# Kernel tuning notes

Hardware: AMD Instinct MI355X
Metric: run time of the kernel (lower is better)

Reference implementation:

```python
import jax, jax.numpy as jnp
import numpy as np

K = 2          # kernel_size
DEPTH = 4
NQ = 4         # n_qubits = max(K*K, DEPTH)
B, C, H, W = 32, 3, 128, 128
LAYERS = 4     # circuit_layers


def setup_inputs() -> dict:
    key = jax.random.key(0)
    k1, k2 = jax.random.split(key)
    x = jax.random.uniform(k1, (B, C, H, W), dtype=jnp.float32)
    # TorchLayer default init is uniform in [0, 2*pi)
    weights = jax.random.uniform(k2, (LAYERS, NQ), dtype=jnp.float32) * (2.0 * np.pi)
    return {"x": x, "weights": weights}


def _apply_ry(state, theta, q):
    # state: [N,2,2,2,2] real amplitudes; theta: scalar; RY = [[c,-s],[s,c]], c=cos(t/2), s=sin(t/2)
    c = jnp.cos(theta / 2)
    s = jnp.sin(theta / 2)
    ax = 1 + q
    a0 = jnp.take(state, 0, axis=ax)
    a1 = jnp.take(state, 1, axis=ax)
    return jnp.stack([c * a0 - s * a1, s * a0 + c * a1], axis=ax)


def _cnot(state, ctrl, tgt):
    # flip target axis on the control=1 slab
    ca, ta = 1 + ctrl, 1 + tgt
    s0 = jnp.take(state, 0, axis=ca)
    s1 = jnp.take(state, 1, axis=ca)
    ta2 = ta - 1 if ta > ca else ta  # axis shift after take removed ca
    s1 = jnp.flip(s1, axis=ta2)
    return jnp.stack([s0, s1], axis=ca)


def reference(x, weights):
    Bx, Cx, Hx, Wx = x.shape
    R = Hx - K + 1  # output spatial size (H == W)
    # 2x2 patches flattened row-major, matching t.reshape(1,-1).squeeze()
    pat = jnp.stack([
        x[:, :, 0:R, 0:R], x[:, :, 0:R, 1:R + 1],
        x[:, :, 1:R + 1, 0:R], x[:, :, 1:R + 1, 1:R + 1],
    ], axis=-1)  # [B,C,R,R,4]
    half = (np.pi * pat).reshape(-1, NQ) / 2  # RY(pi*x)/2 encoding angles, [N,4]
    amp = jnp.stack([jnp.cos(half), jnp.sin(half)], axis=-1)  # [N,4,2]
    # product state over 4 qubits -> [N,2,2,2,2]
    state = jnp.einsum('na,nb,nc,nd->nabcd', amp[:, 0], amp[:, 1], amp[:, 2], amp[:, 3])
    # StructureLayer: per layer RY on all wires, then CNOT(0,1), CNOT(2,3), CNOT(1,2)
    for layer in range(weights.shape[0]):
        for q in range(NQ):
            state = _apply_ry(state, weights[layer, q], q)
        state = _cnot(state, 0, 1)
        state = _cnot(state, 2, 3)
        state = _cnot(state, 1, 2)
    probs = state * state  # amplitudes are real
    sgn = jnp.array([1.0, -1.0], dtype=state.dtype)
    z = jnp.stack([
        jnp.einsum('nabcd,a->n', probs, sgn),
        jnp.einsum('nabcd,b->n', probs, sgn),
        jnp.einsum('nabcd,c->n', probs, sgn),
        jnp.einsum('nabcd,d->n', probs, sgn),
    ], axis=-1)  # [N, DEPTH]
    q_out = z.reshape(Bx, Cx, R, R, DEPTH).sum(axis=1)  # sum over channels -> [B,R,R,DEPTH]
    # faithful to torch.reshape (memory reinterpretation, NOT a transpose)
    return q_out.reshape(Bx, DEPTH, R, R)
```

## Files before the change

### kernel.cpp

```cpp
#include <hip/hip_runtime.h>


#define BATCH   32
#define CHAN    3
#define HDIM    128
#define WDIM    128
#define RDIM    127
#define NLAYERS 4

__global__ __launch_bounds__(256) void rqcnn_kernel(
    const float* __restrict__ x,
    const float* __restrict__ w,
    float* __restrict__ out)
{
    __shared__ float cw_s[16], sw_s[16];
    const int t = threadIdx.x;
    if (t < 16) {
        float rev = w[t] * 0.07957747154594767f;
        cw_s[t] = __builtin_amdgcn_cosf(rev);
        sw_s[t] = __builtin_amdgcn_sinf(rev);
    }
    __syncthreads();

    float cw[16], sw[16];
    #pragma unroll
    for (int k = 0; k < 16; ++k) { cw[k] = cw_s[k]; sw[k] = sw_s[k]; }

    const int NPIX = BATCH * RDIM * RDIM;
    int tid = blockIdx.x * 256 + t;
    if (tid >= NPIX) return;

    int j    = tid % RDIM;
    int rest = tid / RDIM;
    int i    = rest % RDIM;
    int b    = rest / RDIM;

    float z0 = 0.f, z1 = 0.f, z2 = 0.f, z3 = 0.f;

    for (int c = 0; c < CHAN; ++c) {
        int base = ((b * CHAN + c) * HDIM + i) * WDIM + j;
        float v0 = x[base];
        float v1 = x[base + 1];
        float v2 = x[base + WDIM];
        float v3 = x[base + WDIM + 1];

        float ca0 = __builtin_amdgcn_cosf(0.25f * v0), sa0 = __builtin_amdgcn_sinf(0.25f * v0);
        float ca1 = __builtin_amdgcn_cosf(0.25f * v1), sa1 = __builtin_amdgcn_sinf(0.25f * v1);
        float ca2 = __builtin_amdgcn_cosf(0.25f * v2), sa2 = __builtin_amdgcn_sinf(0.25f * v2);
        float ca3 = __builtin_amdgcn_cosf(0.25f * v3), sa3 = __builtin_amdgcn_sinf(0.25f * v3);

        float aq[2] = {ca0, sa0};
        float bq[2] = {ca1, sa1};
        float cq[2] = {ca2, sa2};
        float dq[2] = {ca3, sa3};

        float st[16];
        #pragma unroll
        for (int ia = 0; ia < 2; ++ia) {
            #pragma unroll
            for (int ib = 0; ib < 2; ++ib) {
                float ab = aq[ia] * bq[ib];
                #pragma unroll
                for (int ic = 0; ic < 2; ++ic) {
                    float abc = ab * cq[ic];
                    #pragma unroll
                    for (int id = 0; id < 2; ++id)
                        st[ia*8 + ib*4 + ic*2 + id] = abc * dq[id];
                }
            }
        }

        #pragma unroll
        for (int l = 0; l < NLAYERS; ++l) {
            #pragma unroll
            for (int q = 0; q < 4; ++q) {
                float cc = cw[l*4 + q];
                float ss = sw[l*4 + q];
                const int m = 1 << (3 - q);
                #pragma unroll
                for (int s0 = 0; s0 < 16; ++s0) {
                    if (s0 & m) continue;
                    int s1i = s0 | m;
                    float a0 = st[s0], a1 = st[s1i];
                    st[s0]  = cc * a0 - ss * a1;
                    st[s1i] = ss * a0 + cc * a1;
                }
            }
            #pragma unroll
            for (int s0 = 0; s0 < 16; ++s0)
                if ((s0 & 8) && !(s0 & 4)) { float tmp = st[s0]; st[s0] = st[s0|4]; st[s0|4] = tmp; }
            #pragma unroll
            for (int s0 = 0; s0 < 16; ++s0)
                if ((s0 & 2) && !(s0 & 1)) { float tmp = st[s0]; st[s0] = st[s0|1]; st[s0|1] = tmp; }
            #pragma unroll
            for (int s0 = 0; s0 < 16; ++s0)
                if ((s0 & 4) && !(s0 & 2)) { float tmp = st[s0]; st[s0] = st[s0|2]; st[s0|2] = tmp; }
        }

        float p[16];
        #pragma unroll
        for (int s0 = 0; s0 < 16; ++s0) p[s0] = st[s0] * st[s0];

        float A0 = (p[0] + p[1]) + (p[2] + p[3]);
        float A1 = (p[4] + p[5]) + (p[6] + p[7]);
        float A2 = (p[8] + p[9]) + (p[10] + p[11]);
        float A3 = (p[12] + p[13]) + (p[14] + p[15]);
        float B0 = (p[0] + p[4]) + (p[8] + p[12]);
        float B1 = (p[1] + p[5]) + (p[9] + p[13]);
        float B2 = (p[2] + p[6]) + (p[10] + p[14]);
        float B3 = (p[3] + p[7]) + (p[11] + p[15]);
        z0 += (A0 + A1) - (A2 + A3);
        z1 += (A0 + A2) - (A1 + A3);
        z2 += (B0 + B1) - (B2 + B3);
        z3 += (B0 + B2) - (B1 + B3);
    }

    reinterpret_cast<float4*>(out)[tid] = make_float4(z0, z1, z2, z3);
}

extern "C" void kernel_launch(void* const* d_in, const int* in_sizes, int n_in,
                              void* d_out, int out_size, void* d_ws, size_t ws_size,
                              hipStream_t stream) {
    const float* x = (const float*)d_in[0];
    const float* w = (const float*)d_in[1];
    float* out = (float*)d_out;

    const int NPIX = BATCH * RDIM * RDIM;
    int blocks = (NPIX + 255) / 256;
    rqcnn_kernel<<<blocks, 256, 0, stream>>>(x, w, out);
}
```

Before: 78.89 us.

## Fold first RY layer into encoding angles and pack two batches per thread

The first layer's RY rotations act on a product state, so they are absorbed into the encoding angles (angle plus weight/2) and only three layers are applied explicitly. Each thread now handles two pixels from the two batch halves using 2-wide float vectors, so the compiler can emit packed FP32 math (v_pk_fma/mul) and the weight loads are amortized over twice the work. This halves the number of threads and raises register pressure per thread, which may lower occupancy.

```diff
diff --git a/kernel.cpp b/kernel.cpp
--- a/kernel.cpp
+++ b/kernel.cpp
@@ -6,63 +6,80 @@
 #define HDIM    128
 #define WDIM    128
 #define RDIM    127
-#define NLAYERS 4
+#define HALFB   16
+
+typedef float v2 __attribute__((ext_vector_type(2)));
 
 __global__ __launch_bounds__(256) void rqcnn_kernel(
     const float* __restrict__ x,
     const float* __restrict__ w,
     float* __restrict__ out)
 {
-    __shared__ float cw_s[16], sw_s[16];
+    __shared__ float cw_s[16], sw_s[16], wrev_s[4];
     const int t = threadIdx.x;
     if (t < 16) {
         float rev = w[t] * 0.07957747154594767f;
         cw_s[t] = __builtin_amdgcn_cosf(rev);
         sw_s[t] = __builtin_amdgcn_sinf(rev);
+        if (t < 4) wrev_s[t] = rev;
     }
     __syncthreads();
 
-    float cw[16], sw[16];
+    float cw[12], sw[12];
     #pragma unroll
-    for (int k = 0; k < 16; ++k) { cw[k] = cw_s[k]; sw[k] = sw_s[k]; }
+    for (int k = 0; k < 12; ++k) { cw[k] = cw_s[k + 4]; sw[k] = sw_s[k + 4]; }
+    float wr0 = wrev_s[0], wr1 = wrev_s[1], wr2 = wrev_s[2], wr3 = wrev_s[3];
 
-    const int NPIX = BATCH * RDIM * RDIM;
+    const int NHALF = HALFB * RDIM * RDIM;
     int tid = blockIdx.x * 256 + t;
-    if (tid >= NPIX) return;
+    if (tid >= NHALF) return;
 
     int j    = tid % RDIM;
     int rest = tid / RDIM;
     int i    = rest % RDIM;
     int b    = rest / RDIM;
 
-    float z0 = 0.f, z1 = 0.f, z2 = 0.f, z3 = 0.f;
+    const int XOFF = HALFB * CHAN * HDIM * WDIM;
+
+    v2 z0 = 0.f, z1 = 0.f, z2 = 0.f, z3 = 0.f;
 
     for (int c = 0; c < CHAN; ++c) {
         int base = ((b * CHAN + c) * HDIM + i) * WDIM + j;
-        float v0 = x[base];
-        float v1 = x[base + 1];
-        float v2 = x[base + WDIM];
-        float v3 = x[base + WDIM + 1];
+        v2 v0, v1, v2v, v3;
+        v0.x  = x[base];              v0.y  = x[base + XOFF];
+        v1.x  = x[base + 1];          v1.y  = x[base + XOFF + 1];
+        v2v.x = x[base + WDIM];       v2v.y = x[base + XOFF + WDIM];
+        v3.x  = x[base + WDIM + 1];   v3.y  = x[base + XOFF + WDIM + 1];
 
-        float ca0 = __builtin_amdgcn_cosf(0.25f * v0), sa0 = __builtin_amdgcn_sinf(0.25f * v0);
-        float ca1 = __builtin_amdgcn_cosf(0.25f * v1), sa1 = __builtin_amdgcn_sinf(0.25f * v1);
-        float ca2 = __builtin_amdgcn_cosf(0.25f * v2), sa2 = __builtin_amdgcn_sinf(0.25f * v2);
-        float ca3 = __builtin_amdgcn_cosf(0.25f * v3), sa3 = __builtin_amdgcn_sinf(0.25f * v3);
+        v2 a0 = 0.25f * v0 + wr0;
+        v2 a1 = 0.25f * v1 + wr1;
+        v2 a2 = 0.25f * v2v + wr2;
+        v2 a3 = 0.25f * v3 + wr3;
 
-        float aq[2] = {ca0, sa0};
-        float bq[2] = {ca1, sa1};
-        float cq[2] = {ca2, sa2};
-        float dq[2] = {ca3, sa3};
+        v2 ca0, sa0, ca1, sa1, ca2, sa2, ca3, sa3;
+        ca0.x = __builtin_amdgcn_cosf(a0.x); ca0.y = __builtin_amdgcn_cosf(a0.y);
+        sa0.x = __builtin_amdgcn_sinf(a0.x); sa0.y = __builtin_amdgcn_sinf(a0.y);
+        ca1.x = __builtin_amdgcn_cosf(a1.x); ca1.y = __builtin_amdgcn_cosf(a1.y);
+        sa1.x = __builtin_amdgcn_sinf(a1.x); sa1.y = __builtin_amdgcn_sinf(a1.y);
+        ca2.x = __builtin_amdgcn_cosf(a2.x); ca2.y = __builtin_amdgcn_cosf(a2.y);
+        sa2.x = __builtin_amdgcn_sinf(a2.x); sa2.y = __builtin_amdgcn_sinf(a2.y);
+        ca3.x = __builtin_amdgcn_cosf(a3.x); ca3.y = __builtin_amdgcn_cosf(a3.y);
+        sa3.x = __builtin_amdgcn_sinf(a3.x); sa3.y = __builtin_amdgcn_sinf(a3.y);
 
-        float st[16];
+        v2 aq[2] = {ca0, sa0};
+        v2 bq[2] = {ca1, sa1};
+        v2 cq[2] = {ca2, sa2};
+        v2 dq[2] = {ca3, sa3};
+
+        v2 st[16];
         #pragma unroll
         for (int ia = 0; ia < 2; ++ia) {
             #pragma unroll
             for (int ib = 0; ib < 2; ++ib) {
-                float ab = aq[ia] * bq[ib];
+                v2 ab = aq[ia] * bq[ib];
                 #pragma unroll
                 for (int ic = 0; ic < 2; ++ic) {
-                    float abc = ab * cq[ic];
+                    v2 abc = ab * cq[ic];
                     #pragma unroll
                     for (int id = 0; id < 2; ++id)
                         st[ia*8 + ib*4 + ic*2 + id] = abc * dq[id];
@@ -71,7 +88,17 @@
         }
 
         #pragma unroll
-        for (int l = 0; l < NLAYERS; ++l) {
+        for (int s0 = 0; s0 < 16; ++s0)
+            if ((s0 & 8) && !(s0 & 4)) { v2 tmp = st[s0]; st[s0] = st[s0|4]; st[s0|4] = tmp; }
+        #pragma unroll
+        for (int s0 = 0; s0 < 16; ++s0)
+            if ((s0 & 2) && !(s0 & 1)) { v2 tmp = st[s0]; st[s0] = st[s0|1]; st[s0|1] = tmp; }
+        #pragma unroll
+        for (int s0 = 0; s0 < 16; ++s0)
+            if ((s0 & 4) && !(s0 & 2)) { v2 tmp = st[s0]; st[s0] = st[s0|2]; st[s0|2] = tmp; }
+
+        #pragma unroll
+        for (int l = 0; l < 3; ++l) {
             #pragma unroll
             for (int q = 0; q < 4; ++q) {
                 float cc = cw[l*4 + q];
@@ -81,41 +108,42 @@
                 for (int s0 = 0; s0 < 16; ++s0) {
                     if (s0 & m) continue;
                     int s1i = s0 | m;
-                    float a0 = st[s0], a1 = st[s1i];
-                    st[s0]  = cc * a0 - ss * a1;
-                    st[s1i] = ss * a0 + cc * a1;
+                    v2 va = st[s0], vb = st[s1i];
+                    st[s0]  = cc * va - ss * vb;
+                    st[s1i] = ss * va + cc * vb;
                 }
             }
             #pragma unroll
             for (int s0 = 0; s0 < 16; ++s0)
-                if ((s0 & 8) && !(s0 & 4)) { float tmp = st[s0]; st[s0] = st[s0|4]; st[s0|4] = tmp; }
+                if ((s0 & 8) && !(s0 & 4)) { v2 tmp = st[s0]; st[s0] = st[s0|4]; st[s0|4] = tmp; }
             #pragma unroll
             for (int s0 = 0; s0 < 16; ++s0)
-                if ((s0 & 2) && !(s0 & 1)) { float tmp = st[s0]; st[s0] = st[s0|1]; st[s0|1] = tmp; }
+                if ((s0 & 2) && !(s0 & 1)) { v2 tmp = st[s0]; st[s0] = st[s0|1]; st[s0|1] = tmp; }
             #pragma unroll
             for (int s0 = 0; s0 < 16; ++s0)
-                if ((s0 & 4) && !(s0 & 2)) { float tmp = st[s0]; st[s0] = st[s0|2]; st[s0|2] = tmp; }
+                if ((s0 & 4) && !(s0 & 2)) { v2 tmp = st[s0]; st[s0] = st[s0|2]; st[s0|2] = tmp; }
         }
 
-        float p[16];
+        v2 p[16];
         #pragma unroll
         for (int s0 = 0; s0 < 16; ++s0) p[s0] = st[s0] * st[s0];
 
-        float A0 = (p[0] + p[1]) + (p[2] + p[3]);
-        float A1 = (p[4] + p[5]) + (p[6] + p[7]);
-        float A2 = (p[8] + p[9]) + (p[10] + p[11]);
-        float A3 = (p[12] + p[13]) + (p[14] + p[15]);
-        float B0 = (p[0] + p[4]) + (p[8] + p[12]);
-        float B1 = (p[1] + p[5]) + (p[9] + p[13]);
-        float B2 = (p[2] + p[6]) + (p[10] + p[14]);
-        float B3 = (p[3] + p[7]) + (p[11] + p[15]);
+        v2 A0 = (p[0] + p[1]) + (p[2] + p[3]);
+        v2 A1 = (p[4] + p[5]) + (p[6] + p[7]);
+        v2 A2 = (p[8] + p[9]) + (p[10] + p[11]);
+        v2 A3 = (p[12] + p[13]) + (p[14] + p[15]);
+        v2 B0 = (p[0] + p[4]) + (p[8] + p[12]);
+        v2 B1 = (p[1] + p[5]) + (p[9] + p[13]);
+        v2 B2 = (p[2] + p[6]) + (p[10] + p[14]);
+        v2 B3 = (p[3] + p[7]) + (p[11] + p[15]);
         z0 += (A0 + A1) - (A2 + A3);
         z1 += (A0 + A2) - (A1 + A3);
         z2 += (B0 + B1) - (B2 + B3);
         z3 += (B0 + B2) - (B1 + B3);
     }
 
-    reinterpret_cast<float4*>(out)[tid] = make_float4(z0, z1, z2, z3);
+    reinterpret_cast<float4*>(out)[tid]         = make_float4(z0.x, z1.x, z2.x, z3.x);
+    reinterpret_cast<float4*>(out)[tid + NHALF] = make_float4(z0.y, z1.y, z2.y, z3.y);
 }
 
 extern "C" void kernel_launch(void* const* d_in, const int* in_sizes, int n_in,
@@ -125,7 +153,7 @@
     const float* w = (const float*)d_in[1];
     float* out = (float*)d_out;
 
-    const int NPIX = BATCH * RDIM * RDIM;
-    int blocks = (NPIX + 255) / 256;
+    const int NHALF = HALFB * RDIM * RDIM;
+    int blocks = (NHALF + 255) / 256;
     rqcnn_kernel<<<blocks, 256, 0, stream>>>(x, w, out);
 }
```

Result: faster. 70.83 us (-10.2%).
